# Performance work log

Measured on AMD Instinct MI355X. Metric: run time of the kernel, lower is better.

## Reference

```python
import jax, jax.numpy as jnp
import numpy as np

B, T, D_IN = 32768, 25, 4
H = 32    # hidden_dims // 2 (per-LSTM hidden size)
HID = 64  # hidden_dims (MLP head width)
NB = 5    # number of LSTM branches
DROP = 0.4


def _lstm_layer(x_tm, Wih, Whh, b):
    # x_tm: [T, B, D] time-major. Returns all hidden states [T, B, H].
    Bn = x_tm.shape[1]
    h0 = jnp.zeros((Bn, H), x_tm.dtype)

    def step(carry, xt):
        h, c = carry
        gates = xt @ Wih.T + h @ Whh.T + b  # [B, 4H], torch gate order i,f,g,o
        i, f, g, o = jnp.split(gates, 4, axis=-1)
        c = jax.nn.sigmoid(f) * c + jax.nn.sigmoid(i) * jnp.tanh(g)
        h = jax.nn.sigmoid(o) * jnp.tanh(c)
        return (h, c), h

    (_, _), hs = jax.lax.scan(step, (h0, h0), x_tm)
    return hs


def setup_inputs() -> dict:
    key = jax.random.key(0)
    ks = jax.random.split(key, 16)
    s = 1.0 / np.sqrt(H)  # torch LSTM/Linear uniform bound scale
    u = lambda k, shape: jax.random.uniform(k, shape, jnp.float32, -s, s)
    return {
        "x": jax.random.normal(ks[0], (B, T, D_IN), jnp.float32),
        "mask": (jax.random.uniform(ks[1], (B, T, D_IN)) > DROP).astype(jnp.float32),
        # layer 0 of each of the 5 LSTMs (input D_IN -> H)
        "Wih0": u(ks[2], (NB, 4 * H, D_IN)),
        "Whh0": u(ks[3], (NB, 4 * H, H)),
        "bih0": u(ks[4], (NB, 4 * H)),
        "bhh0": u(ks[5], (NB, 4 * H)),
        # layer 1 of each of the 5 LSTMs (H -> H)
        "Wih1": u(ks[6], (NB, 4 * H, H)),
        "Whh1": u(ks[7], (NB, 4 * H, H)),
        "bih1": u(ks[8], (NB, 4 * H)),
        "bhh1": u(ks[9], (NB, 4 * H)),
        # MLP head: Linear(H->HID), GELU, Linear(HID->HID)
        "W1": u(ks[10], (HID, H)),
        "b1": u(ks[11], (HID,)),
        "W2": u(ks[12], (HID, HID)),
        "b2": u(ks[13], (HID,)),
    }


def reference(x, mask, Wih0, Whh0, bih0, bhh0, Wih1, Whh1, bih1, bhh1, W1, b1, W2, b2):
    xm = x * mask  # elementwise input dropout-mask (precomputed binary mask)
    hiddens = []
    for i in range(NB):  # fixed small structural loop over 5 distinct LSTMs
        sub = xm[:, -(i + 1) * 5 :, :]           # [B, 5*(i+1), D_IN]
        sub_tm = jnp.swapaxes(sub, 0, 1)         # time-major [t, B, D_IN]
        hs0 = _lstm_layer(sub_tm, Wih0[i], Whh0[i], bih0[i] + bhh0[i])  # [t,B,H]
        hs1 = _lstm_layer(hs0, Wih1[i], Whh1[i], bih1[i] + bhh1[i])     # [t,B,H]
        hiddens.append(hs1[-1])                  # last-layer final hidden [B,H]
    hidden = jnp.stack(hiddens, axis=1)          # [B, 5, H]
    h = jax.nn.gelu(hidden @ W1.T + b1, approximate=False)  # torch exact GELU
    out = h @ W2.T + b2                          # [B, 5, HID]
    return out
```

## Files before the change

### kernel.cpp

```cpp
#include <hip/hip_runtime.h>
#include <hip/hip_bf16.h>

#define BQ   32768
#define TT   25
#define DIN  4
#define HH   32
#define GG   128
#define NBR  5
#define HIDD 64
#define WPB  8
#define LOG2E    1.4426950408889634f
#define TWOLOG2E 2.8853900817779268f

using bfrag = __attribute__((ext_vector_type(8))) short;
using accf  = __attribute__((ext_vector_type(4))) float;
using f2    = __attribute__((ext_vector_type(2))) float;

__device__ __forceinline__ float fexp2(float x){
#if __has_builtin(__builtin_amdgcn_exp2f)
  return __builtin_amdgcn_exp2f(x);
#else
  return exp2f(x);
#endif
}
__device__ __forceinline__ float frcpf(float x){
#if __has_builtin(__builtin_amdgcn_rcpf)
  return __builtin_amdgcn_rcpf(x);
#else
  return 1.0f / x;
#endif
}
__device__ __forceinline__ unsigned short fb(float f){
  unsigned u = __builtin_bit_cast(unsigned, f);
  u += 0x7fffu + ((u >> 16) & 1u);
  return (unsigned short)(u >> 16);
}
__device__ __forceinline__ bfrag pack8s(const float* p, float s){
  bfrag w;
#pragma unroll
  for (int j = 0; j < 8; ++j) w[j] = (short)fb(p[j] * s);
  return w;
}
__device__ __forceinline__ accf mma(bfrag a, bfrag b, accf c){
  return __builtin_amdgcn_mfma_f32_16x16x32_bf16(a, b, c, 0, 0, 0);
}
__device__ __forceinline__ unsigned cvtpk(f2 h){
  unsigned r;
  asm("v_cvt_pk_bf16_f32 %0, %1, %2" : "=v"(r) : "v"(h.x), "v"(h.y));
  return r;
}

__device__ __forceinline__ f2 cellh2(f2 iv, f2 fv, f2 gv, f2 ov, f2& cs){
  const f2 one = {1.0f, 1.0f};
  f2 ei = {fexp2(-iv.x), fexp2(-iv.y)};
  f2 ef = {fexp2(-fv.x), fexp2(-fv.y)};
  f2 t  = {fexp2(gv.x),  fexp2(gv.y)};
  f2 df = one + ef;
  f2 d1 = (one + ei) * (t + one);
  f2 num = cs * d1 + (f2){TWOLOG2E, TWOLOG2E} * ((t - one) * df);
  f2 den = df * d1;
  float pr = frcpf(den.x * den.y);
  f2 cp = num * (f2){den.y * pr, den.x * pr};
  cp.x = __builtin_amdgcn_fmed3f(cp.x, -40.f, 40.f);
  cp.y = __builtin_amdgcn_fmed3f(cp.y, -40.f, 40.f);
  cs = cp;
  f2 eo = {fexp2(-ov.x), fexp2(-ov.y)};
  f2 tc = {fexp2(cp.x), fexp2(cp.y)};
  f2 d3 = (one + eo) * (tc + one);
  float p3 = frcpf(d3.x * d3.y);
  return (tc - one) * (f2){d3.y * p3, d3.x * p3};
}
template<int RP>
__device__ __forceinline__ f2 mkf2(accf a){ return (f2){a[RP*2], a[RP*2+1]}; }
__device__ __forceinline__ f2 addb(f2 a, float b){ return (f2){a.x + b, a.y + b}; }

#define CELLSTORE(PK, UT, RP) do {                                        \
    unsigned _pk = (PK);                                                  \
    int _b = (quad * 4 + (RP) * 2) * 40 + (UT) * 16 + col;                \
    hb[_b]      = (unsigned short)_pk;                                    \
    hb[_b + 40] = (unsigned short)(_pk >> 16);                            \
  } while (0)

#define SMEM_SH 18432

__global__ __launch_bounds__(512, 4) void lstm_kernel(
    const float* __restrict__ x,    const float* __restrict__ mask,
    const float* __restrict__ Wih0, const float* __restrict__ Whh0,
    const float* __restrict__ bih0, const float* __restrict__ bhh0,
    const float* __restrict__ Wih1, const float* __restrict__ Whh1,
    const float* __restrict__ bih1, const float* __restrict__ bhh1,
    const float* __restrict__ W1,   const float* __restrict__ b1,
    const float* __restrict__ W2,   const float* __restrict__ b2,
    float* __restrict__ out)
{
  __shared__ __align__(16) unsigned short smem[SMEM_SH];
  unsigned short* wB = smem;
  unsigned short* wX = smem + 12288;
  const int tid  = threadIdx.x;
  const int wave = tid >> 6, lane = tid & 63;
  const int col  = lane & 15, quad = lane >> 4;
  const int branch = 4 - (int)(blockIdx.x >> 8);
  const int tile   = (int)(blockIdx.x & 255) * WPB + wave;
  const int batch0 = tile * 16;
  const int L = (branch + 1) * 5, t0 = TT - L;
  unsigned short* hb = smem + 13312 + wave * 640;

  {
    const float* srcs[3] = { Whh0 + branch * GG * HH,
                             Wih1 + branch * GG * HH,
                             Whh1 + branch * GG * HH };
#pragma unroll
    for (int m = 0; m < 3; ++m) {
      const float* src = srcs[m];
#pragma unroll
      for (int i = 0; i < 8; ++i) {
        int v = tid + i * 512;
        float f = src[v];
        int g = v >> 5, k = v & 31;
        float sc = ((g >> 5) == 2) ? TWOLOG2E : LOG2E;
        int nt = g >> 4, cv = g & 15, q = k >> 3, j = k & 7;
        wB[((m * 8 + nt) * 64 + q * 16 + cv) * 8 + j] = fb(f * sc);
      }
    }
    if (tid < 128) {
      int nt = tid >> 4, cv = tid & 15, g = nt * 16 + cv;
      float sc = ((g >> 5) == 2) ? TWOLOG2E : LOG2E;
      const float* q4 = Wih0 + branch * GG * DIN + g * DIN;
      unsigned short* d = wX + tid * 8;
      d[0] = fb(q4[0] * sc); d[1] = fb(q4[1] * sc);
      d[2] = fb(q4[2] * sc); d[3] = fb(q4[3] * sc);
      d[4] = fb((bih0[branch * GG + g] + bhh0[branch * GG + g]) * sc);
      d[5] = 0; d[6] = 0; d[7] = 0;
    }
  }
  float bias1[8];
#pragma unroll
  for (int nt = 0; nt < 8; ++nt) {
    int g = nt * 16 + col;
    float sc = ((g >> 5) == 2) ? TWOLOG2E : LOG2E;
    bias1[nt] = (bih1[branch * GG + g] + bhh1[branch * GG + g]) * sc;
  }
  __syncthreads();

  const accf zacc = {0.f, 0.f, 0.f, 0.f};
  const f2 zf2 = {0.f, 0.f};
  bfrag aH0 = {0,0,0,0,0,0,0,0}, aH1 = {0,0,0,0,0,0,0,0};
  f2 c0[2][2] = {{zf2, zf2}, {zf2, zf2}};
  f2 c1[2][2] = {{zf2, zf2}, {zf2, zf2}};

  const float* xrow = x    + (size_t)(batch0 + col) * (TT * DIN);
  const float* mrow = mask + (size_t)(batch0 + col) * (TT * DIN);
  float4 xv, mv;
  if (quad == 0) {
    xv = *reinterpret_cast<const float4*>(xrow + t0 * 4);
    mv = *reinterpret_cast<const float4*>(mrow + t0 * 4);
  }

  bfrag ax = {0,0,0,0,0,0,0,0};

  for (int s = 0; s < L; ++s) {
    if (quad == 0) {
      union { bfrag f; unsigned u[4]; } axu;
      axu.u[0] = cvtpk((f2){xv.x * mv.x, xv.y * mv.y});
      axu.u[1] = cvtpk((f2){xv.z * mv.z, xv.w * mv.w});
      axu.u[2] = 0x3F80u;
      axu.u[3] = 0u;
      ax = axu.f;
      if (s + 1 < L) {
        xv = *reinterpret_cast<const float4*>(xrow + (t0 + s + 1) * 4);
        mv = *reinterpret_cast<const float4*>(mrow + (t0 + s + 1) * 4);
      }
    }
    accf acc[8];
#pragma unroll
    for (int nt = 0; nt < 8; ++nt) {
      bfrag bx = *reinterpret_cast<const bfrag*>(wX + (nt * 16 + col) * 8);
      acc[nt] = mma(ax, bx, zacc);
    }
#pragma unroll
    for (int nt = 0; nt < 8; ++nt) {
      bfrag bw = *reinterpret_cast<const bfrag*>(wB + ((0 * 8 + nt) * 64 + quad * 16 + col) * 8);
      acc[nt] = mma(aH0, bw, acc[nt]);
    }
    {
      f2 h;
      h = cellh2(mkf2<0>(acc[0]), mkf2<0>(acc[2]), mkf2<0>(acc[4]), mkf2<0>(acc[6]), c0[0][0]);
      CELLSTORE(cvtpk(h), 0, 0);
      h = cellh2(mkf2<1>(acc[0]), mkf2<1>(acc[2]), mkf2<1>(acc[4]), mkf2<1>(acc[6]), c0[0][1]);
      CELLSTORE(cvtpk(h), 0, 1);
      h = cellh2(mkf2<0>(acc[1]), mkf2<0>(acc[3]), mkf2<0>(acc[5]), mkf2<0>(acc[7]), c0[1][0]);
      CELLSTORE(cvtpk(h), 1, 0);
      h = cellh2(mkf2<1>(acc[1]), mkf2<1>(acc[3]), mkf2<1>(acc[5]), mkf2<1>(acc[7]), c0[1][1]);
      CELLSTORE(cvtpk(h), 1, 1);
    }
    aH0 = *reinterpret_cast<const bfrag*>(hb + col * 40 + quad * 8);
#pragma unroll
    for (int nt = 0; nt < 8; ++nt) {
      bfrag bw = *reinterpret_cast<const bfrag*>(wB + ((1 * 8 + nt) * 64 + quad * 16 + col) * 8);
      acc[nt] = mma(aH0, bw, zacc);
    }
#pragma unroll
    for (int nt = 0; nt < 8; ++nt) {
      bfrag bw = *reinterpret_cast<const bfrag*>(wB + ((2 * 8 + nt) * 64 + quad * 16 + col) * 8);
      acc[nt] = mma(aH1, bw, acc[nt]);
    }
    {
      f2 h;
      h = cellh2(addb(mkf2<0>(acc[0]), bias1[0]), addb(mkf2<0>(acc[2]), bias1[2]),
                 addb(mkf2<0>(acc[4]), bias1[4]), addb(mkf2<0>(acc[6]), bias1[6]), c1[0][0]);
      CELLSTORE(cvtpk(h), 0, 0);
      h = cellh2(addb(mkf2<1>(acc[0]), bias1[0]), addb(mkf2<1>(acc[2]), bias1[2]),
                 addb(mkf2<1>(acc[4]), bias1[4]), addb(mkf2<1>(acc[6]), bias1[6]), c1[0][1]);
      CELLSTORE(cvtpk(h), 0, 1);
      h = cellh2(addb(mkf2<0>(acc[1]), bias1[1]), addb(mkf2<0>(acc[3]), bias1[3]),
                 addb(mkf2<0>(acc[5]), bias1[5]), addb(mkf2<0>(acc[7]), bias1[7]), c1[1][0]);
      CELLSTORE(cvtpk(h), 1, 0);
      h = cellh2(addb(mkf2<1>(acc[1]), bias1[1]), addb(mkf2<1>(acc[3]), bias1[3]),
                 addb(mkf2<1>(acc[5]), bias1[5]), addb(mkf2<1>(acc[7]), bias1[7]), c1[1][1]);
      CELLSTORE(cvtpk(h), 1, 1);
    }
    aH1 = *reinterpret_cast<const bfrag*>(hb + col * 40 + quad * 8);
  }

  unsigned short* fcb = hb;
  accf t1[4];
#pragma unroll
  for (int nt = 0; nt < 4; ++nt) {
    const int n = nt * 16 + col;
    bfrag bw1 = pack8s(W1 + n * HH + quad * 8, 1.0f);
    t1[nt] = (accf){b1[n], b1[n], b1[n], b1[n]};
    t1[nt] = mma(aH1, bw1, t1[nt]);
  }
#pragma unroll
  for (int nt = 0; nt < 2; ++nt)
#pragma unroll
    for (int r = 0; r < 4; ++r) {
      float v = t1[nt][r];
      v = 0.5f * v * (1.0f + erff(v * 0.70710678f));
      fcb[(quad * 4 + r) * 40 + nt * 16 + col] = fb(v);
    }
  bfrag af0 = *reinterpret_cast<const bfrag*>(fcb + col * 40 + quad * 8);
#pragma unroll
  for (int nt = 2; nt < 4; ++nt)
#pragma unroll
    for (int r = 0; r < 4; ++r) {
      float v = t1[nt][r];
      v = 0.5f * v * (1.0f + erff(v * 0.70710678f));
      fcb[(quad * 4 + r) * 40 + (nt - 2) * 16 + col] = fb(v);
    }
  bfrag af1 = *reinterpret_cast<const bfrag*>(fcb + col * 40 + quad * 8);
  accf o[4];
#pragma unroll
  for (int nt = 0; nt < 4; ++nt) {
    const int n = nt * 16 + col;
    bfrag bw2a = pack8s(W2 + n * HIDD + quad * 8, 1.0f);
    bfrag bw2b = pack8s(W2 + n * HIDD + 32 + quad * 8, 1.0f);
    o[nt] = (accf){b2[n], b2[n], b2[n], b2[n]};
    o[nt] = mma(af0, bw2a, o[nt]);
    o[nt] = mma(af1, bw2b, o[nt]);
  }
#pragma unroll
  for (int nt = 0; nt < 4; ++nt)
#pragma unroll
    for (int r = 0; r < 4; ++r) {
      const int row = quad * 4 + r;
      out[(size_t)((batch0 + row) * NBR + branch) * HIDD + nt * 16 + col] = o[nt][r];
    }
}

extern "C" void kernel_launch(void* const* d_in, const int* in_sizes, int n_in,
                              void* d_out, int out_size, void* d_ws, size_t ws_size,
                              hipStream_t stream) {
  const float* x    = (const float*)d_in[0];
  const float* mask = (const float*)d_in[1];
  const float* Wih0 = (const float*)d_in[2];
  const float* Whh0 = (const float*)d_in[3];
  const float* bih0 = (const float*)d_in[4];
  const float* bhh0 = (const float*)d_in[5];
  const float* Wih1 = (const float*)d_in[6];
  const float* Whh1 = (const float*)d_in[7];
  const float* bih1 = (const float*)d_in[8];
  const float* bhh1 = (const float*)d_in[9];
  const float* W1   = (const float*)d_in[10];
  const float* b1   = (const float*)d_in[11];
  const float* W2   = (const float*)d_in[12];
  const float* b2   = (const float*)d_in[13];
  float* out = (float*)d_out;

  const int nblocks = (BQ / (16 * WPB)) * NBR;
  lstm_kernel<<<nblocks, 512, 0, stream>>>(x, mask, Wih0, Whh0, bih0, bhh0,
                                           Wih1, Whh1, bih1, bhh1, W1, b1, W2, b2, out);
}
```

Before: 250.7 us.

## Software-pipeline layer-0 gates of next step under layer-1 cell math

Restructures the recurrent loop so the layer-0 gate MMAs for step s+1 are issued before the layer-1 cell nonlinearities of step s, with a scheduling barrier to keep that order. The layer-1 MMAs for step s now start from the h1 term so they do not wait on the fresh h0. The aim is to overlap matrix-core work with transcendental VALU work inside each wave and hide the dependency chain between the two LSTM layers. It needs a second set of accumulators, so launch bounds drop from 4 to 3 waves per SIMD, trading occupancy for more registers.

```diff
diff --git a/kernel.cpp b/kernel.cpp
--- a/kernel.cpp
+++ b/kernel.cpp
@@ -83,7 +83,7 @@
 
 #define SMEM_SH 18432
 
-__global__ __launch_bounds__(512, 4) void lstm_kernel(
+__global__ __launch_bounds__(512, 3) void lstm_kernel(
     const float* __restrict__ x,    const float* __restrict__ mask,
     const float* __restrict__ Wih0, const float* __restrict__ Whh0,
     const float* __restrict__ bih0, const float* __restrict__ bhh0,
@@ -157,85 +157,110 @@
   }
 
   bfrag ax = {0,0,0,0,0,0,0,0};
+  accf acc0[8];
+
+  if (quad == 0) {
+    union { bfrag f; unsigned u[4]; } axu;
+    axu.u[0] = cvtpk((f2){xv.x * mv.x, xv.y * mv.y});
+    axu.u[1] = cvtpk((f2){xv.z * mv.z, xv.w * mv.w});
+    axu.u[2] = 0x3F80u;
+    axu.u[3] = 0u;
+    ax = axu.f;
+    if (L > 1) {
+      xv = *reinterpret_cast<const float4*>(xrow + (t0 + 1) * 4);
+      mv = *reinterpret_cast<const float4*>(mrow + (t0 + 1) * 4);
+    }
+  }
+#pragma unroll
+  for (int nt = 0; nt < 8; ++nt) {
+    bfrag bx = *reinterpret_cast<const bfrag*>(wX + (nt * 16 + col) * 8);
+    acc0[nt] = mma(ax, bx, zacc);
+  }
 
   for (int s = 0; s < L; ++s) {
-    if (quad == 0) {
-      union { bfrag f; unsigned u[4]; } axu;
-      axu.u[0] = cvtpk((f2){xv.x * mv.x, xv.y * mv.y});
-      axu.u[1] = cvtpk((f2){xv.z * mv.z, xv.w * mv.w});
-      axu.u[2] = 0x3F80u;
-      axu.u[3] = 0u;
-      ax = axu.f;
-      if (s + 1 < L) {
-        xv = *reinterpret_cast<const float4*>(xrow + (t0 + s + 1) * 4);
-        mv = *reinterpret_cast<const float4*>(mrow + (t0 + s + 1) * 4);
-      }
-    }
-    accf acc[8];
-#pragma unroll
-    for (int nt = 0; nt < 8; ++nt) {
-      bfrag bx = *reinterpret_cast<const bfrag*>(wX + (nt * 16 + col) * 8);
-      acc[nt] = mma(ax, bx, zacc);
-    }
-#pragma unroll
-    for (int nt = 0; nt < 8; ++nt) {
-      bfrag bw = *reinterpret_cast<const bfrag*>(wB + ((0 * 8 + nt) * 64 + quad * 16 + col) * 8);
-      acc[nt] = mma(aH0, bw, acc[nt]);
-    }
     {
       f2 h;
-      h = cellh2(mkf2<0>(acc[0]), mkf2<0>(acc[2]), mkf2<0>(acc[4]), mkf2<0>(acc[6]), c0[0][0]);
+      h = cellh2(mkf2<0>(acc0[0]), mkf2<0>(acc0[2]), mkf2<0>(acc0[4]), mkf2<0>(acc0[6]), c0[0][0]);
       CELLSTORE(cvtpk(h), 0, 0);
-      h = cellh2(mkf2<1>(acc[0]), mkf2<1>(acc[2]), mkf2<1>(acc[4]), mkf2<1>(acc[6]), c0[0][1]);
+      h = cellh2(mkf2<1>(acc0[0]), mkf2<1>(acc0[2]), mkf2<1>(acc0[4]), mkf2<1>(acc0[6]), c0[0][1]);
       CELLSTORE(cvtpk(h), 0, 1);
-      h = cellh2(mkf2<0>(acc[1]), mkf2<0>(acc[3]), mkf2<0>(acc[5]), mkf2<0>(acc[7]), c0[1][0]);
+      h = cellh2(mkf2<0>(acc0[1]), mkf2<0>(acc0[3]), mkf2<0>(acc0[5]), mkf2<0>(acc0[7]), c0[1][0]);
       CELLSTORE(cvtpk(h), 1, 0);
-      h = cellh2(mkf2<1>(acc[1]), mkf2<1>(acc[3]), mkf2<1>(acc[5]), mkf2<1>(acc[7]), c0[1][1]);
+      h = cellh2(mkf2<1>(acc0[1]), mkf2<1>(acc0[3]), mkf2<1>(acc0[5]), mkf2<1>(acc0[7]), c0[1][1]);
       CELLSTORE(cvtpk(h), 1, 1);
     }
     aH0 = *reinterpret_cast<const bfrag*>(hb + col * 40 + quad * 8);
+
+    accf t1[8];
+#pragma unroll
+    for (int nt = 0; nt < 8; ++nt) {
+      bfrag bw = *reinterpret_cast<const bfrag*>(wB + ((2 * 8 + nt) * 64 + quad * 16 + col) * 8);
+      t1[nt] = mma(aH1, bw, zacc);
+    }
 #pragma unroll
     for (int nt = 0; nt < 8; ++nt) {
       bfrag bw = *reinterpret_cast<const bfrag*>(wB + ((1 * 8 + nt) * 64 + quad * 16 + col) * 8);
-      acc[nt] = mma(aH0, bw, zacc);
-    }
-#pragma unroll
-    for (int nt = 0; nt < 8; ++nt) {
-      bfrag bw = *reinterpret_cast<const bfrag*>(wB + ((2 * 8 + nt) * 64 + quad * 16 + col) * 8);
-      acc[nt] = mma(aH1, bw, acc[nt]);
-    }
+      t1[nt] = mma(aH0, bw, t1[nt]);
+    }
+
+    if (s + 1 < L) {
+      if (quad == 0) {
+        union { bfrag f; unsigned u[4]; } axu;
+        axu.u[0] = cvtpk((f2){xv.x * mv.x, xv.y * mv.y});
+        axu.u[1] = cvtpk((f2){xv.z * mv.z, xv.w * mv.w});
+        axu.u[2] = 0x3F80u;
+        axu.u[3] = 0u;
+        ax = axu.f;
+        if (s + 2 < L) {
+          xv = *reinterpret_cast<const float4*>(xrow + (t0 + s + 2) * 4);
+          mv = *reinterpret_cast<const float4*>(mrow + (t0 + s + 2) * 4);
+        }
+      }
+#pragma unroll
+      for (int nt = 0; nt < 8; ++nt) {
+        bfrag bx = *reinterpret_cast<const bfrag*>(wX + (nt * 16 + col) * 8);
+        acc0[nt] = mma(ax, bx, zacc);
+      }
+#pragma unroll
+      for (int nt = 0; nt < 8; ++nt) {
+        bfrag bw = *reinterpret_cast<const bfrag*>(wB + ((0 * 8 + nt) * 64 + quad * 16 + col) * 8);
+        acc0[nt] = mma(aH0, bw, acc0[nt]);
+      }
+    }
+    __builtin_amdgcn_sched_barrier(0);
+
     {
       f2 h;
-      h = cellh2(addb(mkf2<0>(acc[0]), bias1[0]), addb(mkf2<0>(acc[2]), bias1[2]),
-                 addb(mkf2<0>(acc[4]), bias1[4]), addb(mkf2<0>(acc[6]), bias1[6]), c1[0][0]);
+      h = cellh2(addb(mkf2<0>(t1[0]), bias1[0]), addb(mkf2<0>(t1[2]), bias1[2]),
+                 addb(mkf2<0>(t1[4]), bias1[4]), addb(mkf2<0>(t1[6]), bias1[6]), c1[0][0]);
       CELLSTORE(cvtpk(h), 0, 0);
-      h = cellh2(addb(mkf2<1>(acc[0]), bias1[0]), addb(mkf2<1>(acc[2]), bias1[2]),
-                 addb(mkf2<1>(acc[4]), bias1[4]), addb(mkf2<1>(acc[6]), bias1[6]), c1[0][1]);
+      h = cellh2(addb(mkf2<1>(t1[0]), bias1[0]), addb(mkf2<1>(t1[2]), bias1[2]),
+                 addb(mkf2<1>(t1[4]), bias1[4]), addb(mkf2<1>(t1[6]), bias1[6]), c1[0][1]);
       CELLSTORE(cvtpk(h), 0, 1);
-      h = cellh2(addb(mkf2<0>(acc[1]), bias1[1]), addb(mkf2<0>(acc[3]), bias1[3]),
-                 addb(mkf2<0>(acc[5]), bias1[5]), addb(mkf2<0>(acc[7]), bias1[7]), c1[1][0]);
+      h = cellh2(addb(mkf2<0>(t1[1]), bias1[1]), addb(mkf2<0>(t1[3]), bias1[3]),
+                 addb(mkf2<0>(t1[5]), bias1[5]), addb(mkf2<0>(t1[7]), bias1[7]), c1[1][0]);
       CELLSTORE(cvtpk(h), 1, 0);
-      h = cellh2(addb(mkf2<1>(acc[1]), bias1[1]), addb(mkf2<1>(acc[3]), bias1[3]),
-                 addb(mkf2<1>(acc[5]), bias1[5]), addb(mkf2<1>(acc[7]), bias1[7]), c1[1][1]);
+      h = cellh2(addb(mkf2<1>(t1[1]), bias1[1]), addb(mkf2<1>(t1[3]), bias1[3]),
+                 addb(mkf2<1>(t1[5]), bias1[5]), addb(mkf2<1>(t1[7]), bias1[7]), c1[1][1]);
       CELLSTORE(cvtpk(h), 1, 1);
     }
     aH1 = *reinterpret_cast<const bfrag*>(hb + col * 40 + quad * 8);
   }
 
   unsigned short* fcb = hb;
-  accf t1[4];
+  accf t1h[4];
 #pragma unroll
   for (int nt = 0; nt < 4; ++nt) {
     const int n = nt * 16 + col;
     bfrag bw1 = pack8s(W1 + n * HH + quad * 8, 1.0f);
-    t1[nt] = (accf){b1[n], b1[n], b1[n], b1[n]};
-    t1[nt] = mma(aH1, bw1, t1[nt]);
+    t1h[nt] = (accf){b1[n], b1[n], b1[n], b1[n]};
+    t1h[nt] = mma(aH1, bw1, t1h[nt]);
   }
 #pragma unroll
   for (int nt = 0; nt < 2; ++nt)
 #pragma unroll
     for (int r = 0; r < 4; ++r) {
-      float v = t1[nt][r];
+      float v = t1h[nt][r];
       v = 0.5f * v * (1.0f + erff(v * 0.70710678f));
       fcb[(quad * 4 + r) * 40 + nt * 16 + col] = fb(v);
     }
@@ -244,7 +269,7 @@
   for (int nt = 2; nt < 4; ++nt)
 #pragma unroll
     for (int r = 0; r < 4; ++r) {
-      float v = t1[nt][r];
+      float v = t1h[nt][r];
       v = 0.5f * v * (1.0f + erff(v * 0.70710678f));
       fcb[(quad * 4 + r) * 40 + (nt - 2) * 16 + col] = fb(v);
     }
```

New measurement: 268.4 us. +7.1%, slower.
